# Kernel tuning notes

Measured on AMD Instinct MI355X. Metric: run time of the kernel, lower is better.

The kernel has to match this reference:

```python
import jax, jax.numpy as jnp
import numpy as np

K_STEPS = 2  # number of staged propagation levels encoded in edge_mask


def _propagate(h, src, dst, mask, num_nodes):
    """KPropagate: K staged scatter-add steps over the edge list.

    Step k sums messages along edges with edge_mask == k; later steps
    propagate the freshly aggregated values (rule-node fan-out).
    """
    out = jnp.zeros_like(h)
    cur = h
    for k in range(K_STEPS):
        msg = jnp.where((mask == k)[:, None], cur[src], jnp.zeros((), h.dtype))  # [E, F]
        out = out + jax.ops.segment_sum(msg, dst, num_segments=num_nodes)
        cur = out
    return out


def setup_inputs() -> dict:
    key = jax.random.key(0)
    ks = jax.random.split(key, 8)
    V, R = 50000, 10000
    N = V + R
    E = 160000
    F_IN, F_OUT = 512, 128
    x = jax.random.normal(ks[0], (N, F_IN), dtype=jnp.float32)
    edge_index = jax.random.randint(ks[1], (2, E), 0, N, dtype=jnp.int64)
    edge_mask = jax.random.randint(ks[2], (E,), 0, K_STEPS, dtype=jnp.int64)
    # lin1: in_features -> in_features; lin2: in_features -> out_features
    s1 = 1.0 / np.sqrt(F_IN)
    W1 = jax.random.uniform(ks[3], (F_IN, F_IN), jnp.float32, -s1, s1)
    b1 = jax.random.uniform(ks[4], (F_IN,), jnp.float32, -s1, s1)
    W2 = jax.random.uniform(ks[5], (F_IN, F_OUT), jnp.float32, -s1, s1)
    b2 = jax.random.uniform(ks[6], (F_OUT,), jnp.float32, -s1, s1)
    return {"x": x, "edge_index": edge_index, "edge_mask": edge_mask,
            "vertex_cnt": V, "rule_cnt": R,
            "W1": W1, "b1": b1, "W2": W2, "b2": b2}


def reference(x, edge_index, edge_mask, vertex_cnt, rule_cnt, W1, b1, W2, b2):
    N = x.shape[0]  # == vertex_cnt + rule_cnt
    src, dst = edge_index[0], edge_index[1]
    h = x @ W1 + b1                                   # lin1
    h = jax.nn.relu(_propagate(h, src, dst, edge_mask, N))  # P1 -> relu
    h = h @ W2 + b2                                   # lin2
    h = _propagate(h, src, dst, edge_mask, N)         # P2
    # NOTE: original code computes log_softmax into `out` but returns x (=h).
    return h
```

## Files before the change

kernel.cpp:

```cpp
#include <hip/hip_runtime.h>

typedef __bf16 bf16x8 __attribute__((ext_vector_type(8)));
typedef float  floatx4 __attribute__((ext_vector_type(4)));
typedef unsigned short ushortx8 __attribute__((ext_vector_type(8)));
typedef unsigned short ushortx4 __attribute__((ext_vector_type(4)));
typedef unsigned short ushortx2 __attribute__((ext_vector_type(2)));

__device__ __forceinline__ float bf2f(unsigned short u) {
    return __uint_as_float(((unsigned)u) << 16);
}
__device__ __forceinline__ unsigned short f2bf(float f) {
    unsigned u = __float_as_uint(f);
    return (unsigned short)((u + 0x7FFFu + ((u >> 16) & 1u)) >> 16);
}

__device__ __forceinline__ void gload_lds16(const unsigned short* g, unsigned short* l) {
    __builtin_amdgcn_global_load_lds(
        (const __attribute__((address_space(1))) void*)g,
        (__attribute__((address_space(3))) void*)l, 16, 0, 0);
}

__global__ void cvt_f32_bf16_kernel(const float* __restrict__ in,
                                    unsigned short* __restrict__ out, int n4) {
    int i = blockIdx.x * blockDim.x + threadIdx.x;
    if (i >= n4) return;
    float4 v = ((const float4*)in)[i];
    ushortx4 o;
    o[0] = f2bf(v.x); o[1] = f2bf(v.y); o[2] = f2bf(v.z); o[3] = f2bf(v.w);
    ((ushortx4*)out)[i] = o;
}

__global__ void transpose_cvt_kernel(const float* __restrict__ in,
                                     unsigned short* __restrict__ out,
                                     int K, int N) {
    int idx = blockIdx.x * blockDim.x + threadIdx.x;
    if (idx >= K * N) return;
    int k = idx / N, n = idx - k * N;
    out[n * K + k] = f2bf(in[idx]);
}

__global__ void init_head_kernel(int* __restrict__ head, int n) {
    int i = blockIdx.x * blockDim.x + threadIdx.x;
    if (i < n) head[i] = -1;
}

__global__ void build_list_kernel(const int* __restrict__ ei, const int* __restrict__ em,
                                  int E, int Nn,
                                  int* __restrict__ head, int* __restrict__ nxt) {
    int e = blockIdx.x * blockDim.x + threadIdx.x;
    if (e >= E) return;
    int d = ei[E + e];
    int m = em[e];
    nxt[e] = atomicExch(&head[m * Nn + d], e);
}

#define BM 128
#define BN 128
#define BK 64

__global__ __launch_bounds__(256) void gemm_bt_bias(
    const unsigned short* __restrict__ A,
    const unsigned short* __restrict__ Bt,
    const float* __restrict__ bias,
    unsigned short* __restrict__ C,
    int M, int N, int K)
{
    __shared__ unsigned short Sh[16384];
    unsigned short (*As)[512] = (unsigned short(*)[512])Sh;
    unsigned short (*Bs)[512] = (unsigned short(*)[512])(Sh + 8192);

    const int tid  = threadIdx.x;
    const int lane = tid & 63;
    const int wave = tid >> 6;

    int bx, by;
    if (gridDim.x == 4) {
        int id = blockIdx.y * 4 + blockIdx.x;
        int full = (gridDim.y & ~7) * 4;
        if (id < full) {
            bx = (id >> 3) & 3;
            by = (id >> 5) * 8 + (id & 7);
        } else {
            int t = id - full;
            by = (gridDim.y & ~7) + (t >> 2);
            bx = t & 3;
        }
    } else {
        bx = blockIdx.x; by = blockIdx.y;
    }
    const int bM = by * BM;
    const int bN = bx * BN;
    const int wm = (wave >> 1) * 64;
    const int wn = (wave & 1) * 64;
    const int q    = lane >> 4;
    const int mrow = lane & 15;

    const unsigned short* pA[4];
    const unsigned short* pB[4];
#pragma unroll
    for (int c = 0; c < 4; c++) {
        int gg = wave + 4 * c;
        int g7 = gg & 7, s = gg >> 3;
        int rA = bM + g7 * 16 + mrow; if (rA >= M) rA = M - 1;
        int rB = bN + g7 * 16 + mrow;
        pA[c] = A  + (size_t)rA * K + s * 32 + q * 8;
        pB[c] = Bt + (size_t)rB * K + s * 32 + q * 8;
    }

    floatx4 acc[4][4];
#pragma unroll
    for (int i = 0; i < 4; i++)
#pragma unroll
        for (int j = 0; j < 4; j++) acc[i][j] = (floatx4)(0.0f);

    for (int kt = 0; kt < K; kt += BK) {
#pragma unroll
        for (int c = 0; c < 4; c++) {
            gload_lds16(pA[c] + kt, &As[wave + 4 * c][0]);
            gload_lds16(pB[c] + kt, &Bs[wave + 4 * c][0]);
        }
        __syncthreads();

#pragma unroll
        for (int s = 0; s < 2; s++) {
            bf16x8 af[4], bfv[4];
#pragma unroll
            for (int mi = 0; mi < 4; mi++)
                af[mi] = *(const bf16x8*)&As[s * 8 + (wave >> 1) * 4 + mi][lane * 8];
#pragma unroll
            for (int ni = 0; ni < 4; ni++)
                bfv[ni] = *(const bf16x8*)&Bs[s * 8 + (wave & 1) * 4 + ni][lane * 8];
#pragma unroll
            for (int mi = 0; mi < 4; mi++)
#pragma unroll
                for (int ni = 0; ni < 4; ni++)
                    acc[mi][ni] = __builtin_amdgcn_mfma_f32_16x16x32_bf16(
                        af[mi], bfv[ni], acc[mi][ni], 0, 0, 0);
        }
        __syncthreads();
    }

    unsigned short* lbuf = Sh + wave * 2048;
    float bv[4];
#pragma unroll
    for (int ni = 0; ni < 4; ni++) bv[ni] = bias[bN + wn + ni * 16 + mrow];

#pragma unroll
    for (int p = 0; p < 2; p++) {
#pragma unroll
        for (int mh = 0; mh < 2; mh++) {
            int mi = 2 * p + mh;
#pragma unroll
            for (int ni = 0; ni < 4; ni++)
#pragma unroll
                for (int r = 0; r < 4; r++)
                    lbuf[(mh * 16 + q * 4 + r) * 64 + ni * 16 + mrow] =
                        f2bf(acc[mi][ni][r] + bv[ni]);
        }
#pragma unroll
        for (int i = 0; i < 4; i++) {
            int prow = i * 8 + (lane >> 3);
            int pcol = (lane & 7) * 8;
            int grow = bM + wm + p * 32 + prow;
            if (grow < M)
                *(ushortx8*)(C + (size_t)grow * N + bN + wn + pcol) =
                    *(const ushortx8*)&lbuf[prow * 64 + pcol];
        }
    }
}

template <int VEC> struct VecT;
template <> struct VecT<8> { typedef ushortx8 type; };
template <> struct VecT<2> { typedef ushortx2 type; };

template <int VEC, bool ADD_SELF, bool RELU, bool OUT_F32>
__global__ __launch_bounds__(256) void prop_step_kernel(
    const unsigned short* __restrict__ cur,
    void* __restrict__ outp,
    const int* __restrict__ head,
    const int* __restrict__ nxt,
    const int* __restrict__ esrc,
    int Nn)
{
    typedef typename VecT<VEC>::type VT;
    const int w = blockIdx.x * 4 + (threadIdx.x >> 6);
    if (w >= Nn) return;
    const int lane = threadIdx.x & 63;
    const int F = VEC * 64;
    const size_t off = (size_t)w * F + lane * VEC;

    float acc[VEC];
    if (ADD_SELF) {
        VT v = *(const VT*)(cur + off);
#pragma unroll
        for (int i = 0; i < VEC; i++) acc[i] = bf2f(v[i]);
    } else {
#pragma unroll
        for (int i = 0; i < VEC; i++) acc[i] = 0.0f;
    }

    for (int e = head[w]; e >= 0; e = nxt[e]) {
        int s = esrc[e];
        VT v = *(const VT*)(cur + (size_t)s * F + lane * VEC);
#pragma unroll
        for (int i = 0; i < VEC; i++) acc[i] += bf2f(v[i]);
    }

#pragma unroll
    for (int i = 0; i < VEC; i++)
        if (RELU && acc[i] < 0.0f) acc[i] = 0.0f;

    if (OUT_F32) {
        float* out = (float*)outp;
        float2 o2;
#pragma unroll
        for (int i = 0; i < VEC; i += 2) {
            o2.x = acc[i]; o2.y = acc[i + 1];
            *(float2*)(out + off + i) = o2;
        }
    } else {
        VT o;
#pragma unroll
        for (int i = 0; i < VEC; i++) o[i] = f2bf(acc[i]);
        *(VT*)((unsigned short*)outp + off) = o;
    }
}

extern "C" void kernel_launch(void* const* d_in, const int* in_sizes, int n_in,
                              void* d_out, int out_size, void* d_ws, size_t ws_size,
                              hipStream_t stream)
{
    const float* x  = (const float*)d_in[0];
    const int*   ei = (const int*)d_in[1];
    const int*   em = (const int*)d_in[2];
    const float* W1 = (const float*)d_in[5];
    const float* b1 = (const float*)d_in[6];
    const float* W2 = (const float*)d_in[7];
    const float* b2 = (const float*)d_in[8];

    const int FIN = 512, FOUT = 128;
    const int Nn = in_sizes[0] / FIN;
    const int E  = in_sizes[2];

    char* ws = (char*)d_ws;
    size_t off = 0;
    auto alloc = [&](size_t bytes) -> char* {
        char* p = ws + off;
        off += (bytes + 255) & ~(size_t)255;
        return p;
    };
    unsigned short* W1t = (unsigned short*)alloc((size_t)FIN * FIN * 2);
    unsigned short* W2t = (unsigned short*)alloc((size_t)FIN * FOUT * 2);
    unsigned short* xb  = (unsigned short*)alloc((size_t)Nn * FIN * 2);
    unsigned short* h1  = (unsigned short*)alloc((size_t)Nn * FIN * 2);
    unsigned short* h2  = (unsigned short*)alloc((size_t)Nn * FOUT * 2);
    unsigned short* A2  = (unsigned short*)alloc((size_t)Nn * FOUT * 2);
    int* head = (int*)alloc((size_t)2 * Nn * 4);
    int* nxt  = (int*)alloc((size_t)E * 4);
    unsigned short* A1 = xb;
    (void)ws_size; (void)n_in; (void)out_size;

    cvt_f32_bf16_kernel<<<((Nn * FIN / 4) + 255) / 256, 256, 0, stream>>>(x, xb, Nn * FIN / 4);
    transpose_cvt_kernel<<<(FIN * FIN + 255) / 256, 256, 0, stream>>>(W1, W1t, FIN, FIN);
    transpose_cvt_kernel<<<(FIN * FOUT + 255) / 256, 256, 0, stream>>>(W2, W2t, FIN, FOUT);

    init_head_kernel<<<(2 * Nn + 255) / 256, 256, 0, stream>>>(head, 2 * Nn);
    build_list_kernel<<<(E + 255) / 256, 256, 0, stream>>>(ei, em, E, Nn, head, nxt);

    {
        dim3 grid(FIN / BN, (Nn + BM - 1) / BM);
        gemm_bt_bias<<<grid, 256, 0, stream>>>(xb, W1t, b1, h1, Nn, FIN, FIN);
    }

    {
        int grid = (Nn + 3) / 4;
        prop_step_kernel<8, false, false, false><<<grid, 256, 0, stream>>>(h1, A1, head,      nxt, ei, Nn);
        prop_step_kernel<8, true,  true,  false><<<grid, 256, 0, stream>>>(A1, h1, head + Nn, nxt, ei, Nn);
    }

    {
        dim3 grid(FOUT / BN, (Nn + BM - 1) / BM);
        gemm_bt_bias<<<grid, 256, 0, stream>>>(h1, W2t, b2, h2, Nn, FOUT, FIN);
    }

    {
        int grid = (Nn + 3) / 4;
        prop_step_kernel<2, false, false, false><<<grid, 256, 0, stream>>>(h2, A2, head,      nxt, ei, Nn);
        prop_step_kernel<2, true,  false, true ><<<grid, 256, 0, stream>>>(A2, d_out, head + Nn, nxt, ei, Nn);
    }
}
```

Before: 398.3 us.

## Pre-stage GEMM operands in tile-contiguous layout for linear LDS loads

```diff
diff --git a/kernel.cpp b/kernel.cpp
--- a/kernel.cpp
+++ b/kernel.cpp
@@ -20,23 +20,39 @@
         (__attribute__((address_space(3))) void*)l, 16, 0, 0);
 }
 
-__global__ void cvt_f32_bf16_kernel(const float* __restrict__ in,
-                                    unsigned short* __restrict__ out, int n4) {
+
+#define NKT 8
+
+__device__ __forceinline__ size_t staged_chunk(int r, int c ) {
+    int tile = r >> 7, rt = r & 127;
+    int g = rt >> 4, mrow = rt & 15;
+    int kti = c >> 3, c7 = c & 7;
+    int s = c7 >> 2, q = c7 & 3;
+    return (((size_t)tile * NKT + kti) << 13) + ((size_t)(s * 8 + g) << 9)
+         + ((size_t)((q << 4) | mrow) << 3);
+}
+
+__global__ void cvt_f32_bf16_staged_kernel(const float* __restrict__ in,
+                                           unsigned short* __restrict__ out,
+                                           int nchunk) {
     int i = blockIdx.x * blockDim.x + threadIdx.x;
-    if (i >= n4) return;
-    float4 v = ((const float4*)in)[i];
-    ushortx4 o;
-    o[0] = f2bf(v.x); o[1] = f2bf(v.y); o[2] = f2bf(v.z); o[3] = f2bf(v.w);
-    ((ushortx4*)out)[i] = o;
-}
-
-__global__ void transpose_cvt_kernel(const float* __restrict__ in,
-                                     unsigned short* __restrict__ out,
-                                     int K, int N) {
+    if (i >= nchunk) return;
+    int r = i >> 6, c = i & 63;
+    float4 v0 = ((const float4*)in)[i * 2];
+    float4 v1 = ((const float4*)in)[i * 2 + 1];
+    ushortx8 o;
+    o[0] = f2bf(v0.x); o[1] = f2bf(v0.y); o[2] = f2bf(v0.z); o[3] = f2bf(v0.w);
+    o[4] = f2bf(v1.x); o[5] = f2bf(v1.y); o[6] = f2bf(v1.z); o[7] = f2bf(v1.w);
+    *(ushortx8*)(out + staged_chunk(r, c)) = o;
+}
+
+__global__ void transpose_cvt_staged_kernel(const float* __restrict__ in,
+                                            unsigned short* __restrict__ out,
+                                            int K, int N) {
     int idx = blockIdx.x * blockDim.x + threadIdx.x;
     if (idx >= K * N) return;
     int k = idx / N, n = idx - k * N;
-    out[n * K + k] = f2bf(in[idx]);
+    out[staged_chunk(n, k >> 3) + (k & 7)] = f2bf(in[idx]);
 }
 
 __global__ void init_head_kernel(int* __restrict__ head, int n) {
@@ -56,9 +72,8 @@
 
 #define BM 128
 #define BN 128
-#define BK 64
-
-__global__ __launch_bounds__(256) void gemm_bt_bias(
+
+__global__ __launch_bounds__(256, 4) void gemm_bt_bias(
     const unsigned short* __restrict__ A,
     const unsigned short* __restrict__ Bt,
     const float* __restrict__ bias,
@@ -95,17 +110,8 @@
     const int q    = lane >> 4;
     const int mrow = lane & 15;
 
-    const unsigned short* pA[4];
-    const unsigned short* pB[4];
-#pragma unroll
-    for (int c = 0; c < 4; c++) {
-        int gg = wave + 4 * c;
-        int g7 = gg & 7, s = gg >> 3;
-        int rA = bM + g7 * 16 + mrow; if (rA >= M) rA = M - 1;
-        int rB = bN + g7 * 16 + mrow;
-        pA[c] = A  + (size_t)rA * K + s * 32 + q * 8;
-        pB[c] = Bt + (size_t)rB * K + s * 32 + q * 8;
-    }
+    const unsigned short* as_ = A  + (((size_t)by * NKT) << 13) + (wave << 11) + (lane << 3);
+    const unsigned short* bs_ = Bt + (((size_t)bx * NKT) << 13) + (wave << 11) + (lane << 3);
 
     floatx4 acc[4][4];
 #pragma unroll
@@ -113,11 +119,11 @@
 #pragma unroll
         for (int j = 0; j < 4; j++) acc[i][j] = (floatx4)(0.0f);
 
-    for (int kt = 0; kt < K; kt += BK) {
+    for (int t = 0; t < NKT; ++t) {
 #pragma unroll
         for (int c = 0; c < 4; c++) {
-            gload_lds16(pA[c] + kt, &As[wave + 4 * c][0]);
-            gload_lds16(pB[c] + kt, &Bs[wave + 4 * c][0]);
+            gload_lds16(as_ + (c << 9), Sh + (wave << 11) + (c << 9));
+            gload_lds16(bs_ + (c << 9), Sh + 8192 + (wave << 11) + (c << 9));
         }
         __syncthreads();
 
@@ -138,6 +144,7 @@
                         af[mi], bfv[ni], acc[mi][ni], 0, 0, 0);
         }
         __syncthreads();
+        as_ += 8192; bs_ += 8192;
     }
 
     unsigned short* lbuf = Sh + wave * 2048;
@@ -173,7 +180,7 @@
 template <> struct VecT<8> { typedef ushortx8 type; };
 template <> struct VecT<2> { typedef ushortx2 type; };
 
-template <int VEC, bool ADD_SELF, bool RELU, bool OUT_F32>
+template <int VEC, bool ADD_SELF, bool RELU, bool OUT_F32, bool OUT_STAGED = false>
 __global__ __launch_bounds__(256) void prop_step_kernel(
     const unsigned short* __restrict__ cur,
     void* __restrict__ outp,
@@ -222,7 +229,11 @@
         VT o;
 #pragma unroll
         for (int i = 0; i < VEC; i++) o[i] = f2bf(acc[i]);
-        *(VT*)((unsigned short*)outp + off) = o;
+        if (OUT_STAGED && VEC == 8) {
+            *(VT*)((unsigned short*)outp + staged_chunk(w, lane)) = o;
+        } else {
+            *(VT*)((unsigned short*)outp + off) = o;
+        }
     }
 }
 
@@ -241,6 +252,7 @@
     const int FIN = 512, FOUT = 128;
     const int Nn = in_sizes[0] / FIN;
     const int E  = in_sizes[2];
+    const int Mpad = ((Nn + 127) >> 7) << 7;
 
     char* ws = (char*)d_ws;
     size_t off = 0;
@@ -251,8 +263,8 @@
     };
     unsigned short* W1t = (unsigned short*)alloc((size_t)FIN * FIN * 2);
     unsigned short* W2t = (unsigned short*)alloc((size_t)FIN * FOUT * 2);
-    unsigned short* xb  = (unsigned short*)alloc((size_t)Nn * FIN * 2);
-    unsigned short* h1  = (unsigned short*)alloc((size_t)Nn * FIN * 2);
+    unsigned short* xb  = (unsigned short*)alloc((size_t)Mpad * FIN * 2);
+    unsigned short* h1  = (unsigned short*)alloc((size_t)Mpad * FIN * 2);
     unsigned short* h2  = (unsigned short*)alloc((size_t)Nn * FOUT * 2);
     unsigned short* A2  = (unsigned short*)alloc((size_t)Nn * FOUT * 2);
     int* head = (int*)alloc((size_t)2 * Nn * 4);
@@ -260,26 +272,29 @@
     unsigned short* A1 = xb;
     (void)ws_size; (void)n_in; (void)out_size;
 
-    cvt_f32_bf16_kernel<<<((Nn * FIN / 4) + 255) / 256, 256, 0, stream>>>(x, xb, Nn * FIN / 4);
-    transpose_cvt_kernel<<<(FIN * FIN + 255) / 256, 256, 0, stream>>>(W1, W1t, FIN, FIN);
-    transpose_cvt_kernel<<<(FIN * FOUT + 255) / 256, 256, 0, stream>>>(W2, W2t, FIN, FOUT);
+    {
+        int nchunk = Nn * (FIN / 8);
+        cvt_f32_bf16_staged_kernel<<<(nchunk + 255) / 256, 256, 0, stream>>>(x, xb, nchunk);
+    }
+    transpose_cvt_staged_kernel<<<(FIN * FIN + 255) / 256, 256, 0, stream>>>(W1, W1t, FIN, FIN);
+    transpose_cvt_staged_kernel<<<(FIN * FOUT + 255) / 256, 256, 0, stream>>>(W2, W2t, FIN, FOUT);
 
     init_head_kernel<<<(2 * Nn + 255) / 256, 256, 0, stream>>>(head, 2 * Nn);
     build_list_kernel<<<(E + 255) / 256, 256, 0, stream>>>(ei, em, E, Nn, head, nxt);
 
     {
-        dim3 grid(FIN / BN, (Nn + BM - 1) / BM);
+        dim3 grid(FIN / BN, Mpad / BM);
         gemm_bt_bias<<<grid, 256, 0, stream>>>(xb, W1t, b1, h1, Nn, FIN, FIN);
     }
 
     {
         int grid = (Nn + 3) / 4;
-        prop_step_kernel<8, false, false, false><<<grid, 256, 0, stream>>>(h1, A1, head,      nxt, ei, Nn);
-        prop_step_kernel<8, true,  true,  false><<<grid, 256, 0, stream>>>(A1, h1, head + Nn, nxt, ei, Nn);
-    }
-
-    {
-        dim3 grid(FOUT / BN, (Nn + BM - 1) / BM);
+        prop_step_kernel<8, false, false, false, false><<<grid, 256, 0, stream>>>(h1, A1, head,      nxt, ei, Nn);
+        prop_step_kernel<8, true,  true,  false, true ><<<grid, 256, 0, stream>>>(A1, h1, head + Nn, nxt, ei, Nn);
+    }
+
+    {
+        dim3 grid(FOUT / BN, Mpad / BM);
         gemm_bt_bias<<<grid, 256, 0, stream>>>(h1, W2t, b2, h2, Nn, FOUT, FIN);
     }
 
```

Result: no change. 391.8 us (-1.6%).
